# Optimization experiments

Hardware: AMD Instinct MI355X
Metric: run time of the kernel (lower is better)

The kernel has to match this reference:

```python
import jax, jax.numpy as jnp
import numpy as np

N_HEADS = 8
N_LAYERS = 2
LN_EPS = 1e-5


def _mha(x, Win, bin_, Wout, bout):
    # torch nn.MultiheadAttention, eval mode (dropout off). x: [b, s, d]
    b, s, d = x.shape
    dh = d // N_HEADS
    qkv = x @ Win.T + bin_                      # [b, s, 3d]
    q, k, v = jnp.split(qkv, 3, axis=-1)
    q = q.reshape(b, s, N_HEADS, dh)
    k = k.reshape(b, s, N_HEADS, dh)
    v = v.reshape(b, s, N_HEADS, dh)
    scores = jnp.einsum('bqhd,bkhd->bhqk', q, k) / jnp.sqrt(jnp.asarray(dh, x.dtype))
    attn = jax.nn.softmax(scores, axis=-1)
    o = jnp.einsum('bhqk,bkhd->bqhd', attn, v).reshape(b, s, d)
    return o @ Wout.T + bout


def _layer_norm(x, g, b):
    mu = jnp.mean(x, axis=-1, keepdims=True)
    var = jnp.mean(jnp.square(x - mu), axis=-1, keepdims=True)
    return (x - mu) * jax.lax.rsqrt(var + LN_EPS) * g + b


def _vertex_conv(feat, inc, prev, Win, bin_, Wout, bout, Wproj, ln_g, ln_b, alpha):
    # feat: [b,m,d], inc: [b,m,e]
    attn = _mha(feat, Win, bin_, Wout, bout)              # [b,m,d]
    scores = jnp.einsum('bme,bmd->bed', inc, attn)        # incidence aggregation
    w = jax.nn.softmax(scores, axis=1)                    # softmax over edges
    # fused form of einsum('bme,bmd->bmed') then einsum('bmed,bed->bed')
    edge = scores * w                                     # [b,e,d]
    edge = edge @ Wproj.T                                 # no-bias projection
    edge = _layer_norm(edge, ln_g, ln_b)
    if prev is not None:
        edge = alpha * prev + (1.0 - alpha) * edge
        edge = edge + prev
    return edge


def _edge_conv(inc, edge_feat, prev, Win, bin_, Wout, bout, Wproj, ln_g, ln_b, alpha):
    # inc: [b,m,e], edge_feat: [b,e,d]
    _ = _mha(edge_feat, Win, bin_, Wout, bout)            # attn computed, output unused downstream
    wef = jnp.einsum('bed,bme->bmd', edge_feat, inc)      # edge->node aggregation
    node = wef @ Wproj.T
    node = _layer_norm(node, ln_g, ln_b)
    if prev is not None:
        node = alpha * prev + (1.0 - alpha) * node
        node = node + prev
    return node


def setup_inputs() -> dict:
    key = jax.random.key(0)
    ks = jax.random.split(key, 8)
    b, m, e, d = 8, 1024, 1536, 256
    s = 0.02
    return {
        'features': jax.random.normal(ks[0], (b, m, d), jnp.float32),
        'inc_mat': (jax.random.uniform(ks[1], (b, m, e), jnp.float32) < 0.05).astype(jnp.float32),
        'vc_Win': jax.random.normal(ks[2], (3 * d, d), jnp.float32) * s,
        'vc_bin': jnp.zeros((3 * d,), jnp.float32),
        'vc_Wout': jax.random.normal(ks[3], (d, d), jnp.float32) * s,
        'vc_bout': jnp.zeros((d,), jnp.float32),
        'vc_Wproj': jax.random.normal(ks[4], (d, d), jnp.float32) * s,
        'vc_ln_g': jnp.ones((d,), jnp.float32),
        'vc_ln_b': jnp.zeros((d,), jnp.float32),
        'vc_alpha': jnp.asarray(0.5, jnp.float32),
        'ec_Win': jax.random.normal(ks[5], (3 * d, d), jnp.float32) * s,
        'ec_bin': jnp.zeros((3 * d,), jnp.float32),
        'ec_Wout': jax.random.normal(ks[6], (d, d), jnp.float32) * s,
        'ec_bout': jnp.zeros((d,), jnp.float32),
        'ec_Wproj': jax.random.normal(ks[7], (d, d), jnp.float32) * s,
        'ec_ln_g': jnp.ones((d,), jnp.float32),
        'ec_ln_b': jnp.zeros((d,), jnp.float32),
        'ec_alpha': jnp.asarray(0.5, jnp.float32),
    }


def reference(features, inc_mat,
              vc_Win, vc_bin, vc_Wout, vc_bout, vc_Wproj, vc_ln_g, vc_ln_b, vc_alpha,
              ec_Win, ec_bin, ec_Wout, ec_bout, ec_Wproj, ec_ln_g, ec_ln_b, ec_alpha):
    vc = (vc_Win, vc_bin, vc_Wout, vc_bout, vc_Wproj, vc_ln_g, vc_ln_b, vc_alpha)
    ec = (ec_Win, ec_bin, ec_Wout, ec_bout, ec_Wproj, ec_ln_g, ec_ln_b, ec_alpha)
    edge_feats = _vertex_conv(features, inc_mat, None, *vc)
    node_feats = _edge_conv(inc_mat, edge_feats, features, *ec)
    for _ in range(N_LAYERS):  # shared weights across layers, as in the torch module
        edge_feats = _vertex_conv(features, inc_mat, edge_feats, *vc)
        node_feats = _edge_conv(inc_mat, edge_feats, node_feats, *ec)
    return node_feats, edge_feats, inc_mat
```

## Files before the change

kernel.cpp:

```cpp
#include <hip/hip_runtime.h>
#include <stdint.h>


#define DEV static __device__ __forceinline__

typedef __attribute__((ext_vector_type(8))) short bf16x8;
typedef __attribute__((ext_vector_type(4))) float f32x4;

DEV uint16_t f2bf(float x){
  union{float f; uint32_t u;} v; v.f=x;
  uint32_t r = v.u + 0x7fffu + ((v.u>>16)&1u);
  return (uint16_t)(r>>16);
}
DEV float bf2f(uint16_t b){
  union{uint32_t u; float f;} v; v.u=((uint32_t)b)<<16; return v.f;
}

#if __has_builtin(__builtin_amdgcn_global_load_lds)
#define HAVE_GLL 1
#else
#define HAVE_GLL 0
#endif

DEV void load_lds16(const uint16_t* g, void* l){
#if HAVE_GLL
  __builtin_amdgcn_global_load_lds((const __attribute__((address_space(1))) uint32_t*)g,
                                   (__attribute__((address_space(3))) uint32_t*)l, 16, 0, 0);
#else
  *(bf16x8*)l = *(const bf16x8*)g;
#endif
}

__global__ __launch_bounds__(256)
void cast_f32_bf16(const float* __restrict__ in, uint16_t* __restrict__ out, int n4){
  int i = blockIdx.x*256 + threadIdx.x;
  if (i < n4){
    float4 v = ((const float4*)in)[i];
    union { uint16_t u[4]; uint64_t q; } p;
    p.u[0]=f2bf(v.x); p.u[1]=f2bf(v.y); p.u[2]=f2bf(v.z); p.u[3]=f2bf(v.w);
    ((uint64_t*)out)[i] = p.q;
  }
}

__global__ __launch_bounds__(256)
void cast_weights(const float* __restrict__ win, const float* __restrict__ wout,
                  const float* __restrict__ wpv, const float* __restrict__ wpe,
                  uint16_t* __restrict__ ow, uint16_t* __restrict__ oo,
                  uint16_t* __restrict__ ov, uint16_t* __restrict__ oe){
  int i = blockIdx.x*256 + threadIdx.x;
  const float* src; uint16_t* dst; int j;
  if (i < 49152){ src=win; dst=ow; j=i; }
  else if (i < 65536){ src=wout; dst=oo; j=i-49152; }
  else if (i < 81920){ src=wpv; dst=ov; j=i-65536; }
  else { src=wpe; dst=oe; j=i-81920; }
  float4 v = ((const float4*)src)[j];
  union { uint16_t u[4]; uint64_t q; } p;
  p.u[0]=f2bf(v.x); p.u[1]=f2bf(v.y); p.u[2]=f2bf(v.z); p.u[3]=f2bf(v.w);
  ((uint64_t*)dst)[j] = p.q;
}

__global__ __launch_bounds__(256)
void prep_inc(const float* __restrict__ inc, float* __restrict__ out_inc,
              uint16_t* __restrict__ incb, uint16_t* __restrict__ incT){
  __shared__ float T[32][33];
  int b = blockIdx.z;
  int c0 = blockIdx.x*32;
  int r0 = blockIdx.y*32;
  int tx = threadIdx.x, ty = threadIdx.y;
  size_t base = (size_t)b*1024*1536;
#pragma unroll
  for (int j=0;j<4;++j){
    int r = r0 + ty + j*8;
    size_t idx = base + (size_t)r*1536 + c0 + tx;
    float v = inc[idx];
    T[ty+j*8][tx] = v;
    out_inc[idx] = v;
    incb[idx] = f2bf(v);
  }
  __syncthreads();
  size_t baseT = (size_t)b*1536*1024;
#pragma unroll
  for (int j=0;j<4;++j){
    int c = c0 + ty + j*8;
    incT[baseT + (size_t)c*1024 + r0 + tx] = f2bf(T[tx][ty+j*8]);
  }
}

__global__ __launch_bounds__(256)
void transpose_cast(const float* __restrict__ in, uint16_t* __restrict__ out,
                    int R, int C){
  __shared__ float T[32][33];
  size_t base = (size_t)blockIdx.z * R * C;
  int c0 = blockIdx.x*32, r0 = blockIdx.y*32;
  int tx = threadIdx.x, ty = threadIdx.y;
#pragma unroll
  for (int j=0;j<4;++j)
    T[ty+j*8][tx] = in[base + (size_t)(r0+ty+j*8)*C + c0 + tx];
  __syncthreads();
#pragma unroll
  for (int j=0;j<4;++j)
    out[base + (size_t)(c0+ty+j*8)*R + r0 + tx] = f2bf(T[tx][ty+j*8]);
}

template<int WM, int BK, int EPI>
__global__ __launch_bounds__(256, 3)
void gemm_nt(const uint16_t* __restrict__ A, const uint16_t* __restrict__ B,
             float* __restrict__ Cf, uint16_t* __restrict__ Cb,
             const float* __restrict__ bias,
             int M, int N, int K, long sA, long sB, long sC,
             float* __restrict__ extra){
  constexpr int AROWS = WM*32;
  constexpr int UPR = BK/8;
  constexpr int RPP = 256/UPR;
  __shared__ short As[AROWS*BK];
  __shared__ short Bs[128*BK];
  const int tid = threadIdx.x;
  const int lane = tid & 63;
  const int w = tid >> 6;
  const int wm = w & 1, wn = w >> 1;
  const int r = lane & 15, q = lane >> 4;
  const long zb = blockIdx.z;
  const uint16_t* Ab = A + zb*sA + (size_t)(blockIdx.x*AROWS)*K;
  const uint16_t* Bb = B + zb*sB + (size_t)(blockIdx.y*128)*K;
  f32x4 acc[WM][4];
#pragma unroll
  for (int i=0;i<WM;++i)
#pragma unroll
    for (int j=0;j<4;++j) acc[i][j] = (f32x4){0.f,0.f,0.f,0.f};

  const int srow = tid / UPR;
  const int sblk = tid % UPR;

  for (int kb = 0; kb < K; kb += BK){
#pragma unroll
    for (int i=0;i<AROWS/RPP;++i){
      int row = srow + RPP*i;
      int lblk = sblk ^ (row & (UPR-1));
      load_lds16(Ab + (size_t)row*K + kb + lblk*8, (char*)As + i*4096 + tid*16);
    }
#pragma unroll
    for (int i=0;i<128/RPP;++i){
      int row = srow + RPP*i;
      int lblk = sblk ^ (row & (UPR-1));
      load_lds16(Bb + (size_t)row*K + kb + lblk*8, (char*)Bs + i*4096 + tid*16);
    }
    __syncthreads();
#pragma unroll
    for (int kc=0;kc<BK/32;++kc){
      bf16x8 af[WM], bf[4];
#pragma unroll
      for (int mt=0;mt<WM;++mt){
        int m = wm*(WM*16) + mt*16 + r;
        af[mt] = *(const bf16x8*)&As[m*BK + ((kc*4 + q) ^ (m&(UPR-1)))*8];
      }
#pragma unroll
      for (int nt=0;nt<4;++nt){
        int n = wn*64 + nt*16 + r;
        bf[nt] = *(const bf16x8*)&Bs[n*BK + ((kc*4 + q) ^ (n&(UPR-1)))*8];
      }
#pragma unroll
      for (int mt=0;mt<WM;++mt)
#pragma unroll
        for (int nt=0;nt<4;++nt)
          acc[mt][nt] = __builtin_amdgcn_mfma_f32_16x16x32_bf16(af[mt], bf[nt], acc[mt][nt], 0,0,0);
    }
    __syncthreads();
  }

  const int gm0 = blockIdx.x*AROWS + wm*(WM*16);
  const int gn0 = blockIdx.y*128 + wn*64;

  if constexpr (EPI == 1){
#pragma unroll
    for (int mt=0;mt<WM;++mt){
      int gmb = gm0 + mt*16 + q*4;
      size_t bb_ = (size_t)(gmb>>10)*(256*1024);
      int mm = gmb & 1023;
#pragma unroll
      for (int nt=0;nt<4;++nt){
        int gn = gn0 + nt*16 + r;
        float bv = bias ? bias[gn] : 0.f;
        union{uint16_t u[4]; uint64_t q64;} pk;
#pragma unroll
        for (int reg=0;reg<4;++reg) pk.u[reg] = f2bf(acc[mt][nt][reg] + bv);
        *(uint64_t*)(Cb + bb_ + (size_t)gn*1024 + mm) = pk.q64;
      }
    }
  } else {
#pragma unroll
    for (int mt=0;mt<WM;++mt){
#pragma unroll
      for (int nt=0;nt<4;++nt){
        int gn = gn0 + nt*16 + r;
        float bv = bias ? bias[gn] : 0.f;
#pragma unroll
        for (int reg=0;reg<4;++reg){
          int gm = gm0 + mt*16 + q*4 + reg;
          float v = acc[mt][nt][reg] + bv;
          size_t off = (size_t)(zb*sC) + (size_t)gm*N + gn;
          if (Cf) Cf[off] = v;
          if (Cb) Cb[off] = f2bf(v);
        }
      }
    }
    if constexpr (EPI == 2){
      __shared__ float colsum[2][128];
#pragma unroll
      for (int nt=0;nt<4;++nt){
        float s = 0.f;
#pragma unroll
        for (int mt=0;mt<WM;++mt)
#pragma unroll
          for (int reg=0;reg<4;++reg) s += __expf(acc[mt][nt][reg]);
        s += __shfl_xor(s, 16);
        s += __shfl_xor(s, 32);
        if (q == 0) colsum[wm][wn*64 + nt*16 + r] = s;
      }
      __syncthreads();
      if (tid < 128){
        float v = colsum[0][tid] + colsum[1][tid];
        extra[((size_t)zb*gridDim.x + blockIdx.x)*256 + blockIdx.y*128 + tid] = v;
      }
    }
  }
}

__global__ __launch_bounds__(256)
void reduce_L(const float* __restrict__ part, float* __restrict__ plinv){
  int b = blockIdx.x, d = threadIdx.x;
  float L = 0.f;
#pragma unroll
  for (int i=0;i<24;++i) L += part[((size_t)b*24 + i)*256 + d];
  plinv[b*256+d] = 1.0f / L;
}

template<int MODE>
__global__ __launch_bounds__(512, 4)
void gemm_ln(const uint16_t* __restrict__ A, const uint16_t* __restrict__ B,
             const float* __restrict__ g, const float* __restrict__ bb,
             const float* __restrict__ alpha, const float* __restrict__ feats,
             float* __restrict__ out, int K){
  __shared__ short As[64*64];
  __shared__ short Bs[256*64];
  __shared__ float lnS[4][64], lnQ[4][64];
  const int tid = threadIdx.x;
  const int lane = tid & 63;
  const int w = tid >> 6;
  const int wm = w & 1;
  const int wn2 = w >> 1;
  const int r = lane & 15, q = lane >> 4;
  const uint16_t* Ab = A + (size_t)(blockIdx.x*64)*K;
  f32x4 acc[2][4];
#pragma unroll
  for (int i=0;i<2;++i)
#pragma unroll
    for (int j=0;j<4;++j) acc[i][j] = (f32x4){0.f,0.f,0.f,0.f};

  const int srow = tid >> 3;
  const int sblk = tid & 7;

  for (int kb = 0; kb < K; kb += 64){
    {
      int row = srow;
      int lblk = sblk ^ (row & 7);
      load_lds16(Ab + (size_t)row*K + kb + lblk*8, (char*)As + tid*16);
    }
#pragma unroll
    for (int i=0;i<4;++i){
      int row = srow + 64*i;
      int lblk = sblk ^ (row & 7);
      load_lds16(B + (size_t)row*K + kb + lblk*8, (char*)Bs + i*8192 + tid*16);
    }
    __syncthreads();
#pragma unroll
    for (int kc=0;kc<2;++kc){
      bf16x8 af[2], bf[4];
#pragma unroll
      for (int mt=0;mt<2;++mt){
        int m = wm*32 + mt*16 + r;
        af[mt] = *(const bf16x8*)&As[m*64 + ((kc*4 + q) ^ (m&7))*8];
      }
#pragma unroll
      for (int nt=0;nt<4;++nt){
        int n = wn2*64 + nt*16 + r;
        bf[nt] = *(const bf16x8*)&Bs[n*64 + ((kc*4 + q) ^ (n&7))*8];
      }
#pragma unroll
      for (int mt=0;mt<2;++mt)
#pragma unroll
        for (int nt=0;nt<4;++nt)
          acc[mt][nt] = __builtin_amdgcn_mfma_f32_16x16x32_bf16(af[mt], bf[nt], acc[mt][nt], 0,0,0);
    }
    __syncthreads();
  }

  float rs[2][4], rq[2][4];
#pragma unroll
  for (int mt=0;mt<2;++mt)
#pragma unroll
    for (int reg=0;reg<4;++reg){
      float s=0.f, s2=0.f;
#pragma unroll
      for (int nt=0;nt<4;++nt){
        float v = acc[mt][nt][reg];
        s += v; s2 += v*v;
      }
#pragma unroll
      for (int off=1; off<16; off<<=1){ s += __shfl_xor(s,off); s2 += __shfl_xor(s2,off); }
      rs[mt][reg]=s; rq[mt][reg]=s2;
    }
  if (r == 0){
#pragma unroll
    for (int mt=0;mt<2;++mt)
#pragma unroll
      for (int reg=0;reg<4;++reg){
        int row = wm*32 + mt*16 + q*4 + reg;
        lnS[wn2][row] = rs[mt][reg];
        lnQ[wn2][row] = rq[mt][reg];
      }
  }
  __syncthreads();

  const float a = alpha[0];
  float c0, c1;
  if constexpr (MODE == 0){ c0 = 3.0f + a; c1 = 0.f; }
  else {
    float ap1 = 1.f + a;
    c0 = (1.f - a)*(ap1*ap1 + ap1 + 1.f);
    c1 = ap1*ap1*ap1;
  }

#pragma unroll
  for (int mt=0;mt<2;++mt){
#pragma unroll
    for (int reg=0;reg<4;++reg){
      int row = wm*32 + mt*16 + q*4 + reg;
      float S = lnS[0][row]+lnS[1][row]+lnS[2][row]+lnS[3][row];
      float Q = lnQ[0][row]+lnQ[1][row]+lnQ[2][row]+lnQ[3][row];
      float mu = S * (1.f/256.f);
      float var = fmaxf(Q*(1.f/256.f) - mu*mu, 0.f);
      float rstd = rsqrtf(var + 1e-5f);
      size_t gm = (size_t)blockIdx.x*64 + row;
#pragma unroll
      for (int nt=0;nt<4;++nt){
        int gn = wn2*64 + nt*16 + r;
        float nv = (acc[mt][nt][reg]-mu)*rstd*g[gn] + bb[gn];
        float o;
        if constexpr (MODE == 0) o = nv * c0;
        else                     o = c1*feats[gm*256+gn] + c0*nv;
        out[gm*256 + gn] = o;
      }
    }
  }
}

DEV void stage_K(short* Kl, const uint16_t* __restrict__ qkv, size_t rowbase,
                 int c, int h, int kr){
  const uint16_t* kp = qkv + ((rowbase + c*256 + kr)*768 + 256 + h*32);
  int sz = (kr&3) ^ ((kr>>2)&1);
#pragma unroll
  for (int lb=0; lb<4; ++lb){
    bf16x8 v = *(const bf16x8*)(kp + lb*8);
    *(bf16x8*)&Kl[kr*32 + ((lb ^ sz))*8] = v;
  }
}

DEV void stage_V(short* VT, const uint16_t* __restrict__ qkv, size_t rowbase,
                 int c, int h, int t){
  int kvp = (t>>1)*2;
  int dhh = (t&1)*16;
  const uint16_t* v0 = qkv + ((rowbase + c*256 + kvp)*768 + 512 + h*32 + dhh);
  const uint16_t* v1 = v0 + 768;
  bf16x8 a0 = *(const bf16x8*)(v0);
  bf16x8 a1 = *(const bf16x8*)(v0+8);
  bf16x8 b0 = *(const bf16x8*)(v1);
  bf16x8 b1 = *(const bf16x8*)(v1+8);
  int blkbase = kvp>>3, off = kvp&7;
#pragma unroll
  for (int i=0;i<8;++i){
    int dh = dhh + i;
    uint32_t pack = (uint32_t)(uint16_t)a0[i] | ((uint32_t)(uint16_t)b0[i]<<16);
    *(uint32_t*)&VT[dh*256 + ((blkbase ^ (dh&7))*8) + off] = pack;
  }
#pragma unroll
  for (int i=0;i<8;++i){
    int dh = dhh + 8 + i;
    uint32_t pack = (uint32_t)(uint16_t)a1[i] | ((uint32_t)(uint16_t)b1[i]<<16);
    *(uint32_t*)&VT[dh*256 + ((blkbase ^ (dh&7))*8) + off] = pack;
  }
}

__global__ __launch_bounds__(512)
void attn_fwd(const uint16_t* __restrict__ qkv, uint16_t* __restrict__ O){
  __shared__ short Kl[256*32];
  __shared__ short VT[32*256];
  __shared__ short Pl[8][32*36];
  const int tid = threadIdx.x, lane = tid&63, w = tid>>6;
  const int r = lane&15, q = lane>>4;
  const int bh = blockIdx.y, b = bh>>3, h = bh&7;
  const int q0 = blockIdx.x*256 + w*32;
  const size_t rowbase = (size_t)b*1024;

  bf16x8 aq[2];
  const float qscale = 0.17677669529663687f;
#pragma unroll
  for (int mt=0;mt<2;++mt){
    const uint16_t* p = qkv + ((rowbase + q0 + mt*16 + r)*768 + h*32 + q*8);
    bf16x8 t = *(const bf16x8*)p;
#pragma unroll
    for (int j=0;j<8;++j)
      t[j] = (short)f2bf(bf2f((uint16_t)t[j]) * qscale);
    aq[mt] = t;
  }

  f32x4 o[2][2];
#pragma unroll
  for (int mt=0;mt<2;++mt){ o[mt][0]=(f32x4){0.f,0.f,0.f,0.f}; o[mt][1]=(f32x4){0.f,0.f,0.f,0.f}; }
  float l[2][4];
#pragma unroll
  for (int mt=0;mt<2;++mt)
#pragma unroll
    for (int reg=0;reg<4;++reg) l[mt][reg] = 0.f;

  for (int c=0;c<4;++c){
    __syncthreads();
    if (tid < 256) stage_K(Kl, qkv, rowbase, c, h, tid);
    else           stage_V(VT, qkv, rowbase, c, h, tid-256);
    __syncthreads();
    for (int s32=0; s32<8; ++s32){
#pragma unroll
      for (int t2=0;t2<2;++t2){
        int rn = s32*32 + t2*16 + r;
        int sz = (rn&3) ^ ((rn>>2)&1);
        bf16x8 bk = *(const bf16x8*)&Kl[rn*32 + ((q ^ sz))*8];
#pragma unroll
        for (int mt=0;mt<2;++mt){
          f32x4 z = (f32x4){0.f,0.f,0.f,0.f};
          f32x4 s = __builtin_amdgcn_mfma_f32_16x16x32_bf16(aq[mt], bk, z, 0,0,0);
#pragma unroll
          for (int reg=0;reg<4;++reg){
            float p = __expf(s[reg]);
            l[mt][reg] += p;
            Pl[w][(mt*16 + q*4 + reg)*36 + t2*16 + r] = (short)f2bf(p);
          }
        }
      }
      bf16x8 bv[2];
#pragma unroll
      for (int db=0;db<2;++db){
        int dh = db*16 + r;
        bv[db] = *(const bf16x8*)&VT[dh*256 + (((s32*4 + q) ^ (dh&7)))*8];
      }
#pragma unroll
      for (int mt=0;mt<2;++mt){
        bf16x8 ap = *(const bf16x8*)&Pl[w][(mt*16 + r)*36 + q*8];
#pragma unroll
        for (int db=0;db<2;++db)
          o[mt][db] = __builtin_amdgcn_mfma_f32_16x16x32_bf16(ap, bv[db], o[mt][db], 0,0,0);
      }
    }
  }

#pragma unroll
  for (int mt=0;mt<2;++mt)
#pragma unroll
    for (int reg=0;reg<4;++reg){
      float v = l[mt][reg];
#pragma unroll
      for (int off=1; off<16; off<<=1) v += __shfl_xor(v, off);
      l[mt][reg] = 1.0f / v;
    }
#pragma unroll
  for (int mt=0;mt<2;++mt)
#pragma unroll
    for (int db=0;db<2;++db)
#pragma unroll
      for (int reg=0;reg<4;++reg){
        float v = o[mt][db][reg] * l[mt][reg];
        int qr = q0 + mt*16 + q*4 + reg;
        O[(rowbase + qr)*256 + h*32 + db*16 + r] = f2bf(v);
      }
}

__global__ __launch_bounds__(256)
void edge_sm_apply(const float* __restrict__ scores, const float* __restrict__ plinv,
                   uint16_t* __restrict__ edgeb){
  int b = blockIdx.y;
  int i4 = blockIdx.x*256 + threadIdx.x;
  int e = i4>>6, d4 = (i4&63)*4;
  size_t off = ((size_t)b*1536 + e)*256 + d4;
  float4 v = *(const float4*)(scores + off);
  float4 Li = *(const float4*)(plinv + b*256 + d4);
  union{uint16_t u[4];uint64_t q;} p;
  p.u[0] = f2bf(v.x * __expf(v.x) * Li.x);
  p.u[1] = f2bf(v.y * __expf(v.y) * Li.y);
  p.u[2] = f2bf(v.z * __expf(v.z) * Li.z);
  p.u[3] = f2bf(v.w * __expf(v.w) * Li.w);
  *(uint64_t*)(edgeb + off) = p.q;
}

extern "C" void kernel_launch(void* const* d_in, const int* in_sizes, int n_in,
                              void* d_out, int out_size, void* d_ws, size_t ws_size,
                              hipStream_t stream){
  const float* features = (const float*)d_in[0];
  const float* inc      = (const float*)d_in[1];
  const float* vc_Win   = (const float*)d_in[2];
  const float* vc_bin   = (const float*)d_in[3];
  const float* vc_Wout  = (const float*)d_in[4];
  const float* vc_bout  = (const float*)d_in[5];
  const float* vc_Wproj = (const float*)d_in[6];
  const float* vc_ln_g  = (const float*)d_in[7];
  const float* vc_ln_b  = (const float*)d_in[8];
  const float* vc_alpha = (const float*)d_in[9];
  const float* ec_Wproj = (const float*)d_in[14];
  const float* ec_ln_g  = (const float*)d_in[15];
  const float* ec_ln_b  = (const float*)d_in[16];
  const float* ec_alpha = (const float*)d_in[17];

  float* out = (float*)d_out;
  float* out_node = out;
  float* out_edge = out + 2097152;
  float* out_inc  = out + 5242880;

  char* ws = (char*)d_ws;
  uint16_t* XB    = (uint16_t*)(ws + 0);
  float*    PART  = (float*)   (ws + 0);
  float*    PLINV = (float*)   (ws + 196608);
  uint16_t* WINB  = (uint16_t*)(ws + 4194304);
  uint16_t* WOUTB = (uint16_t*)(ws + 4587520);
  uint16_t* WPVB  = (uint16_t*)(ws + 4718592);
  uint16_t* WPEB  = (uint16_t*)(ws + 4849664);
  uint16_t* INCB  = (uint16_t*)(ws + 4988928);
  uint16_t* INCT  = (uint16_t*)(ws + 30154752);
  uint16_t* QKVB  = (uint16_t*)(ws + 55320576);
  float*    SCORES= (float*)   (ws + 55320576);
  uint16_t* OB    = (uint16_t*)(ws + 67903488);
  uint16_t* ATTNT = (uint16_t*)(ws + 72097792);
  uint16_t* EDGEB = (uint16_t*)(ws + 76292096);
  uint16_t* BASET = (uint16_t*)(ws + 82583552);
  uint16_t* W0B   = (uint16_t*)(ws + 88875008);

  cast_f32_bf16<<<2048,256,0,stream>>>(features, XB, 524288);
  cast_weights<<<384,256,0,stream>>>(vc_Win, vc_Wout, vc_Wproj, ec_Wproj,
                                     WINB, WOUTB, WPVB, WPEB);
  prep_inc<<<dim3(48,32,8), dim3(32,8), 0, stream>>>(inc, out_inc, INCB, INCT);

  gemm_nt<4,64,0><<<dim3(64,6,1),256,0,stream>>>(XB, WINB, nullptr, QKVB, vc_bin,
                                                 8192,768,256, 0,0,0, nullptr);
  attn_fwd<<<dim3(4,64),512,0,stream>>>(QKVB, OB);
  gemm_nt<2,128,1><<<dim3(128,2,1),256,0,stream>>>(OB, WOUTB, nullptr, ATTNT, vc_bout,
                                                   8192,256,256, 0,0,0, nullptr);

  gemm_nt<2,128,2><<<dim3(24,2,8),256,0,stream>>>(INCT, ATTNT, SCORES, nullptr, nullptr,
                                                  1536,256,1024,
                                                  1536L*1024, 256L*1024, 1536L*256, PART);
  reduce_L<<<8,256,0,stream>>>(PART, PLINV);
  edge_sm_apply<<<dim3(384,8),256,0,stream>>>(SCORES, PLINV, EDGEB);

  gemm_ln<0><<<192,512,0,stream>>>(EDGEB, WPVB, vc_ln_g, vc_ln_b, vc_alpha,
                                   nullptr, out_edge, 256);

  transpose_cast<<<dim3(8,48,8), dim3(32,8), 0, stream>>>(out_edge, BASET, 1536, 256);
  gemm_nt<2,128,0><<<dim3(16,2,8),256,0,stream>>>(INCB, BASET, nullptr, W0B, nullptr,
                                                  1024,256,1536,
                                                  1024L*1536, 256L*1536, 1024L*256, nullptr);
  gemm_ln<1><<<128,512,0,stream>>>(W0B, WPEB, ec_ln_g, ec_ln_b, ec_alpha,
                                   features, out_node, 256);
}
```

Before: 280.9 us.

## Fuse cast kernels, fold transpose into LN epilogue, retile attention per wave

Merges the feature and weight bf16 casts into a single launch. Removes the separate transpose_cast pass by having the vertex gemm_ln epilogue write the transposed bf16 edge features directly. Rewrites attn_fwd so each wave handles 16 query rows instead of 32, using a swapped MFMA operand order so probabilities are stored packed, and doubles the grid. The attention change raises parallelism but halves K/V reuse per block staging.

```diff
diff --git a/kernel.cpp b/kernel.cpp
--- a/kernel.cpp
+++ b/kernel.cpp
@@ -32,27 +32,22 @@
 }
 
 __global__ __launch_bounds__(256)
-void cast_f32_bf16(const float* __restrict__ in, uint16_t* __restrict__ out, int n4){
-  int i = blockIdx.x*256 + threadIdx.x;
-  if (i < n4){
-    float4 v = ((const float4*)in)[i];
-    union { uint16_t u[4]; uint64_t q; } p;
-    p.u[0]=f2bf(v.x); p.u[1]=f2bf(v.y); p.u[2]=f2bf(v.z); p.u[3]=f2bf(v.w);
-    ((uint64_t*)out)[i] = p.q;
-  }
-}
-
-__global__ __launch_bounds__(256)
-void cast_weights(const float* __restrict__ win, const float* __restrict__ wout,
-                  const float* __restrict__ wpv, const float* __restrict__ wpe,
-                  uint16_t* __restrict__ ow, uint16_t* __restrict__ oo,
-                  uint16_t* __restrict__ ov, uint16_t* __restrict__ oe){
+void cast_all(const float* __restrict__ feats, const float* __restrict__ win,
+              const float* __restrict__ wout, const float* __restrict__ wpv,
+              const float* __restrict__ wpe,
+              uint16_t* __restrict__ xb, uint16_t* __restrict__ ow,
+              uint16_t* __restrict__ oo, uint16_t* __restrict__ ov,
+              uint16_t* __restrict__ oe){
   int i = blockIdx.x*256 + threadIdx.x;
   const float* src; uint16_t* dst; int j;
-  if (i < 49152){ src=win; dst=ow; j=i; }
-  else if (i < 65536){ src=wout; dst=oo; j=i-49152; }
-  else if (i < 81920){ src=wpv; dst=ov; j=i-65536; }
-  else { src=wpe; dst=oe; j=i-81920; }
+  if (i < 524288){ src=feats; dst=xb; j=i; }
+  else {
+    i -= 524288;
+    if (i < 49152){ src=win; dst=ow; j=i; }
+    else if (i < 65536){ src=wout; dst=oo; j=i-49152; }
+    else if (i < 81920){ src=wpv; dst=ov; j=i-65536; }
+    else { src=wpe; dst=oe; j=i-81920; }
+  }
   float4 v = ((const float4*)src)[j];
   union { uint16_t u[4]; uint64_t q; } p;
   p.u[0]=f2bf(v.x); p.u[1]=f2bf(v.y); p.u[2]=f2bf(v.z); p.u[3]=f2bf(v.w);
@@ -84,22 +79,6 @@
     int c = c0 + ty + j*8;
     incT[baseT + (size_t)c*1024 + r0 + tx] = f2bf(T[tx][ty+j*8]);
   }
-}
-
-__global__ __launch_bounds__(256)
-void transpose_cast(const float* __restrict__ in, uint16_t* __restrict__ out,
-                    int R, int C){
-  __shared__ float T[32][33];
-  size_t base = (size_t)blockIdx.z * R * C;
-  int c0 = blockIdx.x*32, r0 = blockIdx.y*32;
-  int tx = threadIdx.x, ty = threadIdx.y;
-#pragma unroll
-  for (int j=0;j<4;++j)
-    T[ty+j*8][tx] = in[base + (size_t)(r0+ty+j*8)*C + c0 + tx];
-  __syncthreads();
-#pragma unroll
-  for (int j=0;j<4;++j)
-    out[base + (size_t)(c0+ty+j*8)*R + r0 + tx] = f2bf(T[tx][ty+j*8]);
 }
 
 template<int WM, int BK, int EPI>
@@ -239,7 +218,7 @@
 void gemm_ln(const uint16_t* __restrict__ A, const uint16_t* __restrict__ B,
              const float* __restrict__ g, const float* __restrict__ bb,
              const float* __restrict__ alpha, const float* __restrict__ feats,
-             float* __restrict__ out, int K){
+             float* __restrict__ out, uint16_t* __restrict__ baset, int K){
   __shared__ short As[64*64];
   __shared__ short Bs[256*64];
   __shared__ float lnS[4][64], lnQ[4][64];
@@ -330,8 +309,9 @@
     c1 = ap1*ap1*ap1;
   }
 
-#pragma unroll
-  for (int mt=0;mt<2;++mt){
+  float mu_[2][4], rstd_[2][4];
+#pragma unroll
+  for (int mt=0;mt<2;++mt)
 #pragma unroll
     for (int reg=0;reg<4;++reg){
       int row = wm*32 + mt*16 + q*4 + reg;
@@ -339,16 +319,33 @@
       float Q = lnQ[0][row]+lnQ[1][row]+lnQ[2][row]+lnQ[3][row];
       float mu = S * (1.f/256.f);
       float var = fmaxf(Q*(1.f/256.f) - mu*mu, 0.f);
-      float rstd = rsqrtf(var + 1e-5f);
-      size_t gm = (size_t)blockIdx.x*64 + row;
-#pragma unroll
-      for (int nt=0;nt<4;++nt){
-        int gn = wn2*64 + nt*16 + r;
-        float nv = (acc[mt][nt][reg]-mu)*rstd*g[gn] + bb[gn];
+      mu_[mt][reg] = mu;
+      rstd_[mt][reg] = rsqrtf(var + 1e-5f);
+    }
+
+  int bb2 = blockIdx.x / 24;
+  int e0  = (blockIdx.x % 24) * 64 + wm*32;
+
+#pragma unroll
+  for (int mt=0;mt<2;++mt){
+#pragma unroll
+    for (int nt=0;nt<4;++nt){
+      int gn = wn2*64 + nt*16 + r;
+      float gv = g[gn], bv = bb[gn];
+      union{uint16_t u[4]; uint64_t q64;} pk;
+#pragma unroll
+      for (int reg=0;reg<4;++reg){
+        int row = wm*32 + mt*16 + q*4 + reg;
+        size_t gm = (size_t)blockIdx.x*64 + row;
+        float nv = (acc[mt][nt][reg]-mu_[mt][reg])*rstd_[mt][reg]*gv + bv;
         float o;
-        if constexpr (MODE == 0) o = nv * c0;
-        else                     o = c1*feats[gm*256+gn] + c0*nv;
+        if constexpr (MODE == 0){ o = nv * c0; pk.u[reg] = f2bf(o); }
+        else o = c1*feats[gm*256+gn] + c0*nv;
         out[gm*256 + gn] = o;
+      }
+      if constexpr (MODE == 0){
+        int ee = e0 + mt*16 + q*4;
+        *(uint64_t*)(baset + ((size_t)bb2*256 + gn)*1536 + ee) = pk.q64;
       }
     }
   }
@@ -394,33 +391,27 @@
 void attn_fwd(const uint16_t* __restrict__ qkv, uint16_t* __restrict__ O){
   __shared__ short Kl[256*32];
   __shared__ short VT[32*256];
-  __shared__ short Pl[8][32*36];
+  __shared__ short Pl[8][16*36];
   const int tid = threadIdx.x, lane = tid&63, w = tid>>6;
   const int r = lane&15, q = lane>>4;
   const int bh = blockIdx.y, b = bh>>3, h = bh&7;
-  const int q0 = blockIdx.x*256 + w*32;
+  const int q0 = blockIdx.x*128 + w*16;
   const size_t rowbase = (size_t)b*1024;
 
-  bf16x8 aq[2];
-  const float qscale = 0.17677669529663687f;
-#pragma unroll
-  for (int mt=0;mt<2;++mt){
-    const uint16_t* p = qkv + ((rowbase + q0 + mt*16 + r)*768 + h*32 + q*8);
+  bf16x8 aq;
+  {
+    const float qscale = 0.17677669529663687f;
+    const uint16_t* p = qkv + ((rowbase + q0 + r)*768 + h*32 + q*8);
     bf16x8 t = *(const bf16x8*)p;
 #pragma unroll
     for (int j=0;j<8;++j)
       t[j] = (short)f2bf(bf2f((uint16_t)t[j]) * qscale);
-    aq[mt] = t;
-  }
-
-  f32x4 o[2][2];
-#pragma unroll
-  for (int mt=0;mt<2;++mt){ o[mt][0]=(f32x4){0.f,0.f,0.f,0.f}; o[mt][1]=(f32x4){0.f,0.f,0.f,0.f}; }
-  float l[2][4];
-#pragma unroll
-  for (int mt=0;mt<2;++mt)
-#pragma unroll
-    for (int reg=0;reg<4;++reg) l[mt][reg] = 0.f;
+    aq = t;
+  }
+
+  f32x4 o[2];
+  o[0]=(f32x4){0.f,0.f,0.f,0.f}; o[1]=(f32x4){0.f,0.f,0.f,0.f};
+  float l = 0.f;
 
   for (int c=0;c<4;++c){
     __syncthreads();
@@ -433,17 +424,16 @@
         int rn = s32*32 + t2*16 + r;
         int sz = (rn&3) ^ ((rn>>2)&1);
         bf16x8 bk = *(const bf16x8*)&Kl[rn*32 + ((q ^ sz))*8];
-#pragma unroll
-        for (int mt=0;mt<2;++mt){
-          f32x4 z = (f32x4){0.f,0.f,0.f,0.f};
-          f32x4 s = __builtin_amdgcn_mfma_f32_16x16x32_bf16(aq[mt], bk, z, 0,0,0);
-#pragma unroll
-          for (int reg=0;reg<4;++reg){
-            float p = __expf(s[reg]);
-            l[mt][reg] += p;
-            Pl[w][(mt*16 + q*4 + reg)*36 + t2*16 + r] = (short)f2bf(p);
-          }
+        f32x4 z = (f32x4){0.f,0.f,0.f,0.f};
+        f32x4 st = __builtin_amdgcn_mfma_f32_16x16x32_bf16(bk, aq, z, 0,0,0);
+        union{uint16_t u[4]; uint64_t q64;} pk;
+#pragma unroll
+        for (int reg=0;reg<4;++reg){
+          float p = __expf(st[reg]);
+          l += p;
+          pk.u[reg] = f2bf(p);
         }
+        *(uint64_t*)&Pl[w][r*36 + t2*16 + q*4] = pk.q64;
       }
       bf16x8 bv[2];
 #pragma unroll
@@ -451,35 +441,23 @@
         int dh = db*16 + r;
         bv[db] = *(const bf16x8*)&VT[dh*256 + (((s32*4 + q) ^ (dh&7)))*8];
       }
-#pragma unroll
-      for (int mt=0;mt<2;++mt){
-        bf16x8 ap = *(const bf16x8*)&Pl[w][(mt*16 + r)*36 + q*8];
-#pragma unroll
-        for (int db=0;db<2;++db)
-          o[mt][db] = __builtin_amdgcn_mfma_f32_16x16x32_bf16(ap, bv[db], o[mt][db], 0,0,0);
-      }
-    }
-  }
-
-#pragma unroll
-  for (int mt=0;mt<2;++mt)
+      bf16x8 ap = *(const bf16x8*)&Pl[w][r*36 + q*8];
+#pragma unroll
+      for (int db=0;db<2;++db)
+        o[db] = __builtin_amdgcn_mfma_f32_16x16x32_bf16(ap, bv[db], o[db], 0,0,0);
+    }
+  }
+
+  l += __shfl_xor(l, 16);
+  l += __shfl_xor(l, 32);
+#pragma unroll
+  for (int db=0;db<2;++db)
 #pragma unroll
     for (int reg=0;reg<4;++reg){
-      float v = l[mt][reg];
-#pragma unroll
-      for (int off=1; off<16; off<<=1) v += __shfl_xor(v, off);
-      l[mt][reg] = 1.0f / v;
-    }
-#pragma unroll
-  for (int mt=0;mt<2;++mt)
-#pragma unroll
-    for (int db=0;db<2;++db)
-#pragma unroll
-      for (int reg=0;reg<4;++reg){
-        float v = o[mt][db][reg] * l[mt][reg];
-        int qr = q0 + mt*16 + q*4 + reg;
-        O[(rowbase + qr)*256 + h*32 + db*16 + r] = f2bf(v);
-      }
+      float li = __shfl(l, q*4 + reg);
+      int qr = q0 + q*4 + reg;
+      O[(rowbase + qr)*256 + h*32 + db*16 + r] = f2bf(o[db][reg] / li);
+    }
 }
 
 __global__ __launch_bounds__(256)
@@ -540,14 +518,13 @@
   uint16_t* BASET = (uint16_t*)(ws + 82583552);
   uint16_t* W0B   = (uint16_t*)(ws + 88875008);
 
-  cast_f32_bf16<<<2048,256,0,stream>>>(features, XB, 524288);
-  cast_weights<<<384,256,0,stream>>>(vc_Win, vc_Wout, vc_Wproj, ec_Wproj,
-                                     WINB, WOUTB, WPVB, WPEB);
+  cast_all<<<2432,256,0,stream>>>(features, vc_Win, vc_Wout, vc_Wproj, ec_Wproj,
+                                  XB, WINB, WOUTB, WPVB, WPEB);
   prep_inc<<<dim3(48,32,8), dim3(32,8), 0, stream>>>(inc, out_inc, INCB, INCT);
 
   gemm_nt<4,64,0><<<dim3(64,6,1),256,0,stream>>>(XB, WINB, nullptr, QKVB, vc_bin,
                                                  8192,768,256, 0,0,0, nullptr);
-  attn_fwd<<<dim3(4,64),512,0,stream>>>(QKVB, OB);
+  attn_fwd<<<dim3(8,64),512,0,stream>>>(QKVB, OB);
   gemm_nt<2,128,1><<<dim3(128,2,1),256,0,stream>>>(OB, WOUTB, nullptr, ATTNT, vc_bout,
                                                    8192,256,256, 0,0,0, nullptr);
 
@@ -558,12 +535,11 @@
   edge_sm_apply<<<dim3(384,8),256,0,stream>>>(SCORES, PLINV, EDGEB);
 
   gemm_ln<0><<<192,512,0,stream>>>(EDGEB, WPVB, vc_ln_g, vc_ln_b, vc_alpha,
-                                   nullptr, out_edge, 256);
-
-  transpose_cast<<<dim3(8,48,8), dim3(32,8), 0, stream>>>(out_edge, BASET, 1536, 256);
+                                   nullptr, out_edge, BASET, 256);
+
   gemm_nt<2,128,0><<<dim3(16,2,8),256,0,stream>>>(INCB, BASET, nullptr, W0B, nullptr,
                                                   1024,256,1536,
                                                   1024L*1536, 256L*1536, 1024L*256, nullptr);
   gemm_ln<1><<<128,512,0,stream>>>(W0B, WPEB, ec_ln_g, ec_ln_b, ec_alpha,
-                                   features, out_node, 256);
-}
+                                   features, out_node, nullptr, 256);
+}
```

New measurement: 274.2 us. 1.02x faster.
